# Kernel tuning notes

Hardware: AMD Instinct MI355X
Metric: run time of the kernel (lower is better)

Reference implementation:

```python
import jax, jax.numpy as jnp
import numpy as np

N, E, H = 50000, 800000, 128
NUM_NC = 40
NUM_LAYERS = 3


def setup_inputs() -> dict:
    key = jax.random.key(0)
    ks = jax.random.split(key, 16)
    s = 1.0 / np.sqrt(H)
    inp = {
        "x": jax.random.normal(ks[0], (N, H), jnp.float32),
        "edge_index": jax.random.randint(ks[1], (2, E), 0, N, jnp.int64),
        "na_alphas": 0.001 * jax.random.normal(ks[2], (3, 4), jnp.float32),
        "sc_alphas": 0.001 * jax.random.normal(ks[3], (2, 2), jnp.float32),
        "la_alphas": 0.001 * jax.random.normal(ks[4], (1, 3), jnp.float32),
        "lin1_W": s * jax.random.normal(ks[5], (H, H), jnp.float32),
        "lin1_b": jnp.zeros((H,), jnp.float32),
        "gcn_W": s * jax.random.normal(ks[6], (3, H, H), jnp.float32),
        "gcn_b": jnp.zeros((3, H), jnp.float32),
        "sage_Ws": s * jax.random.normal(ks[7], (3, H, H), jnp.float32),
        "sage_Wn": s * jax.random.normal(ks[8], (3, H, H), jnp.float32),
        "gin_W": s * jax.random.normal(ks[9], (3, H, H), jnp.float32),
        "gin_b": jnp.zeros((3, H), jnp.float32),
        "gin_eps": jnp.zeros((3,), jnp.float32),
        "gat_W": s * jax.random.normal(ks[10], (3, H, H), jnp.float32),
        "gat_as": s * jax.random.normal(ks[11], (3, H), jnp.float32),
        "gat_ad": s * jax.random.normal(ks[12], (3, H), jnp.float32),
        "nc_W": s * jax.random.normal(ks[13], (NUM_NC, H), jnp.float32),
        "nc_b": jnp.zeros((NUM_NC,), jnp.float32),
    }
    return inp


def _gcn(x, src, dst, deg_inv_sqrt, W, b):
    h = x @ W.T + b                           # [N, H]
    norm = deg_inv_sqrt[src] * deg_inv_sqrt[dst]
    msg = h[src] * norm[:, None]              # [E, H] gather
    return jax.ops.segment_sum(msg, dst, num_segments=N)


def _sage(x, src, dst, deg, Ws, Wn):
    agg = jax.ops.segment_sum(x[src], dst, num_segments=N) / jnp.maximum(deg, 1.0)[:, None]
    return x @ Ws.T + agg @ Wn.T


def _gin(x, src, dst, W, b, eps):
    agg = jax.ops.segment_sum(x[src], dst, num_segments=N)
    return ((1.0 + eps) * x + agg) @ W.T + b


def _gat(x, src, dst, W, a_s, a_d):
    h = x @ W.T                               # [N, H]
    logits = jax.nn.leaky_relu((h @ a_s)[src] + (h @ a_d)[dst], 0.2)  # [E]
    m = jax.ops.segment_max(logits, dst, num_segments=N)
    e = jnp.exp(logits - m[dst])
    z = jax.ops.segment_sum(e, dst, num_segments=N)
    alpha = e / (z[dst] + 1e-16)
    return jax.ops.segment_sum(alpha[:, None] * h[src], dst, num_segments=N)


def _na_mixed(x, w, src, dst, deg, dis, l, gcn_W, gcn_b, sage_Ws, sage_Wn,
              gin_W, gin_b, gin_eps, gat_W, gat_as, gat_ad):
    # sum_i w_i * elu(op_i(x, edge_index))
    o0 = _gcn(x, src, dst, dis, gcn_W[l], gcn_b[l])
    o1 = _sage(x, src, dst, deg, sage_Ws[l], sage_Wn[l])
    o2 = _gin(x, src, dst, gin_W[l], gin_b[l], gin_eps[l])
    o3 = _gat(x, src, dst, gat_W[l], gat_as[l], gat_ad[l])
    return (w[0] * jax.nn.elu(o0) + w[1] * jax.nn.elu(o1)
            + w[2] * jax.nn.elu(o2) + w[3] * jax.nn.elu(o3))


def reference(x, edge_index, na_alphas, sc_alphas, la_alphas, lin1_W, lin1_b,
              gcn_W, gcn_b, sage_Ws, sage_Wn, gin_W, gin_b, gin_eps,
              gat_W, gat_as, gat_ad, nc_W, nc_b):
    src, dst = edge_index[0], edge_index[1]
    deg = jax.ops.segment_sum(jnp.ones((E,), x.dtype), dst, num_segments=N)
    dis = jnp.where(deg > 0, 1.0 / jnp.sqrt(jnp.maximum(deg, 1.0)), 0.0)

    na_w = jax.nn.softmax(na_alphas, axis=-1)   # [3, 4]
    sc_w = jax.nn.softmax(sc_alphas, axis=-1)   # [2, 2] (none, skip)
    la_w = jax.nn.softmax(la_alphas, axis=-1)   # [1, 3]

    h = x @ lin1_W.T + lin1_b                   # dropout: eval mode -> identity
    xs = []
    cur = h
    for l in range(NUM_LAYERS):
        cur = _na_mixed(cur, na_w[l], src, dst, deg, dis, l, gcn_W, gcn_b,
                        sage_Ws, sage_Wn, gin_W, gin_b, gin_eps,
                        gat_W, gat_as, gat_ad)
        xs.append(cur)
    x1, x2, x3 = xs

    # fix_last=True: x4 = (x3, sc0(x1), sc1(x2)); SC ops = {none->0, skip->id}
    t = jnp.stack([x3, sc_w[0, 1] * x1, sc_w[1, 1] * x2], axis=0)  # [3, N, H]

    # layer aggregator: sum_i w_i * relu(op_i(tuple)); ops = {max, mean, sum}
    x5 = (la_w[0, 0] * jax.nn.relu(jnp.max(t, axis=0))
          + la_w[0, 1] * jax.nn.relu(jnp.mean(t, axis=0))
          + la_w[0, 2] * jax.nn.relu(jnp.sum(t, axis=0)))

    return x5 @ nc_W.T + nc_b                   # [N, NUM_NC]
```

## Files before the change

### kernel.cpp

```cpp
#include <hip/hip_runtime.h>
#include <hip/hip_bf16.h>

typedef unsigned short u16;
typedef unsigned int u32;
typedef __attribute__((ext_vector_type(8))) short short8;
typedef __attribute__((ext_vector_type(4))) float f32x4;
typedef __attribute__((ext_vector_type(2))) float f32x2;

#define HD 128
#define ETILE 8192

__device__ inline float b2f(u16 u){ u32 v = ((u32)u) << 16; return __uint_as_float(v); }
__device__ inline u16 f2b(float f){
  u32 u = __float_as_uint(f);
  u32 r = (u + 0x7fffu + ((u >> 16) & 1u)) >> 16;
  return (u16)r;
}
__device__ inline u32 pack2(float a, float b){
  __hip_bfloat162 h = __float22bfloat162_rn(make_float2(a, b));
  union { __hip_bfloat162 h; u32 u; } c; c.h = h; return c.u;
}
__device__ inline float lo2f(u32 w){ return b2f((u16)(w & 0xffff)); }
__device__ inline float hi2f(u32 w){ return b2f((u16)(w >> 16)); }
__device__ inline float eluf(float x){ return x > 0.f ? x : __expf(x) - 1.f; }
__device__ inline float reluf(float x){ return x > 0.f ? x : 0.f; }
__device__ inline float sane(float x){
  if (!(x == x)) return 0.f;
  return fminf(fmaxf(x, -1e30f), 1e30f);
}
__device__ inline u32 fenc(float f){ u32 u = __float_as_uint(f); return (u & 0x80000000u) ? ~u : (u | 0x80000000u); }
__device__ inline float fdec(u32 u){ return __uint_as_float((u & 0x80000000u) ? (u & 0x7fffffffu) : ~u); }
__device__ __forceinline__ void async16(const u16* g, u16* l){
  __builtin_amdgcn_global_load_lds((const __attribute__((address_space(1))) void*)g,
                                   (__attribute__((address_space(3))) void*)l, 16, 0, 0);
}

__global__ void k_small(const float* __restrict__ na_a, const float* __restrict__ sc_a,
                        const float* __restrict__ la_a, const float* __restrict__ gatW,
                        const float* __restrict__ gat_as, const float* __restrict__ gat_ad,
                        const float* __restrict__ gin_eps, float* __restrict__ sm,
                        u32* __restrict__ maxs)
{
  int t = threadIdx.x;
  if (t < 3) maxs[t] = 0u;
  if (t == 0){
    for (int l = 0; l < 3; l++){
      float a[4]; float mx = -1e30f;
      for (int i = 0; i < 4; i++){ a[i] = na_a[l*4+i]; mx = fmaxf(mx, a[i]); }
      float ssum = 0.f;
      for (int i = 0; i < 4; i++){ a[i] = __expf(a[i]-mx); ssum += a[i]; }
      for (int i = 0; i < 4; i++) sm[l*4+i] = a[i]/ssum;
    }
    for (int r = 0; r < 2; r++){
      float a0 = sc_a[r*2], a1 = sc_a[r*2+1];
      float mx = fmaxf(a0,a1);
      float e0 = __expf(a0-mx), e1 = __expf(a1-mx);
      sm[12+r] = e1/(e0+e1);
    }
    {
      float a0=la_a[0], a1=la_a[1], a2=la_a[2];
      float mx = fmaxf(fmaxf(a0,a1),a2);
      float e0=__expf(a0-mx), e1=__expf(a1-mx), e2=__expf(a2-mx);
      float ssum = e0+e1+e2;
      sm[14]=e0/ssum; sm[15]=e1/ssum; sm[16]=e2/ssum;
    }
    for (int l=0;l<3;l++) sm[17+l] = 1.f + gin_eps[l];
  }
  if (t < 128){
    for (int l=0;l<3;l++){
      float a1=0.f, a2=0.f;
      for (int k=0;k<128;k++){
        float wv = gatW[l*16384 + k*128 + t];
        a1 = fmaf(wv, gat_as[l*128+k], a1);
        a2 = fmaf(wv, gat_ad[l*128+k], a2);
      }
      sm[32  + l*128 + t] = a1;
      sm[416 + l*128 + t] = a2;
    }
  }
}

__device__ __forceinline__ uint4 cvt8(const float* __restrict__ p){
  float4 v0 = *(const float4*)p;
  float4 v1 = *(const float4*)(p + 4);
  uint4 o;
  o.x = pack2(v0.x, v0.y);
  o.y = pack2(v0.z, v0.w);
  o.z = pack2(v1.x, v1.y);
  o.w = pack2(v1.z, v1.w);
  return o;
}
__global__ void k_wcvt(const float* __restrict__ lin1W, const float* __restrict__ gcnW,
                       const float* __restrict__ Ws, const float* __restrict__ Wn,
                       const float* __restrict__ ginW, const float* __restrict__ gatW,
                       u16* __restrict__ wsb)
{
  int i = blockIdx.x*256 + threadIdx.x;
  if (i >= 32768) return;
  int m = i >> 11;
  int j = i & 2047;
  int r = j >> 4, c = j & 15;
  const float* src;
  if (m == 0)       src = lin1W;
  else if (m < 4)   src = gcnW + (m-1)*16384;
  else if (m < 7)   src = Ws   + (m-4)*16384;
  else if (m < 10)  src = Wn   + (m-7)*16384;
  else if (m < 13)  src = ginW + (m-10)*16384;
  else              src = gatW + (m-13)*16384;
  int dj = r*16 + (c ^ (r & 15));
  *(uint4*)(wsb + ((size_t)m*2048 + dj)*8) = cvt8(src + r*HD + c*8);
}


__global__ void k_ehist(const int* __restrict__ ei, int E, int* __restrict__ eh){
  __shared__ int h[256];
  int t = threadIdx.x, b = blockIdx.x;
  h[t] = 0; __syncthreads();
  int base = b*ETILE;
  #pragma unroll
  for (int r = 0; r < ETILE/256; r++){
    int e = base + r*256 + t;
    if (e < E) atomicAdd(&h[ei[E + e] >> 8], 1);
  }
  __syncthreads();
  eh[b*256 + t] = h[t];
}
__global__ void k_escan(int* __restrict__ eh, int nblk, int* __restrict__ btot){
  __shared__ int s[256];
  int b = blockIdx.x, t = threadIdx.x;
  int carry = 0;
  int rounds = (nblk + 255)/256;
  for (int r = 0; r < rounds; r++){
    int i = r*256 + t;
    int v = (i < nblk) ? eh[i*256 + b] : 0;
    s[t] = v; __syncthreads();
    for (int off = 1; off < 256; off <<= 1){
      int a = (t >= off) ? s[t - off] : 0;
      __syncthreads();
      s[t] += a;
      __syncthreads();
    }
    if (i < nblk) eh[i*256 + b] = s[t] - v + carry;
    carry += s[255];
    __syncthreads();
  }
  if (t == 0) btot[b] = carry;
}
__global__ void k_bscan(const int* __restrict__ btot, int B, int E, int* __restrict__ bbase){
  __shared__ int s[256];
  int t = threadIdx.x;
  int v = (t < B) ? btot[t] : 0;
  s[t] = v; __syncthreads();
  for (int off = 1; off < 256; off <<= 1){
    int a = (t >= off) ? s[t - off] : 0;
    __syncthreads();
    s[t] += a;
    __syncthreads();
  }
  if (t < B) bbase[t] = s[t] - v;
  if (t == 0) bbase[B] = E;
}
__global__ void k_escat(const int* __restrict__ ei, int E, int B,
                        const int* __restrict__ eh, const int* __restrict__ bbase,
                        int2* __restrict__ ebuf){
  __shared__ int cur[256];
  int t = threadIdx.x, b = blockIdx.x;
  cur[t] = (t < B) ? bbase[t] + eh[b*256 + t] : 0;
  __syncthreads();
  int base = b*ETILE;
  #pragma unroll
  for (int r = 0; r < ETILE/256; r++){
    int e = base + r*256 + t;
    if (e < E){
      int sv = ei[e], dv = ei[E + e];
      int p = atomicAdd(&cur[dv >> 8], 1);
      ebuf[p] = make_int2(sv, dv);
    }
  }
}
__global__ void k_bcount(const int2* __restrict__ ebuf, const int* __restrict__ bbase,
                         int Nn, int* __restrict__ cnt){
  __shared__ int c[256];
  int t = threadIdx.x, b = blockIdx.x;
  c[t] = 0; __syncthreads();
  int beg = bbase[b], end2 = bbase[b+1];
  for (int i = beg + t; i < end2; i += 256)
    atomicAdd(&c[ebuf[i].y & 255], 1);
  __syncthreads();
  int node = b*256 + t;
  if (node < Nn) cnt[node] = c[t];
}
__global__ void k_bfill(const int2* __restrict__ ebuf, const int* __restrict__ bbase,
                        const int* __restrict__ rowptr, int Nn, int* __restrict__ csr){
  __shared__ int cu[256];
  int t = threadIdx.x, b = blockIdx.x;
  int node = b*256 + t;
  cu[t] = (node < Nn) ? rowptr[node] : 0;
  __syncthreads();
  int beg = bbase[b], end2 = bbase[b+1];
  for (int i = beg + t; i < end2; i += 256){
    int2 ed = ebuf[i];
    int p = atomicAdd(&cu[ed.y & 255], 1);
    csr[p] = ed.x;
  }
}

__global__ void k_scan1(const int* __restrict__ cnt, int Nn, int* __restrict__ bsum){
  __shared__ int red[256];
  int b = blockIdx.x, t = threadIdx.x;
  int base = b*1024 + t*4;
  int s = 0;
  #pragma unroll
  for (int k = 0; k < 4; k++){ int i = base + k; if (i < Nn) s += cnt[i]; }
  red[t] = s; __syncthreads();
  for (int off = 128; off; off >>= 1){
    if (t < off) red[t] += red[t + off];
    __syncthreads();
  }
  if (t == 0) bsum[b] = red[0];
}

__global__ void k_scan2(const int* __restrict__ bsum, int nb,
                        int* __restrict__ boffs, int* __restrict__ rowptr, int Nn){
  __shared__ int sc[1024];
  int t = threadIdx.x;
  int own = (t < nb) ? bsum[t] : 0;
  sc[t] = own;
  __syncthreads();
  for (int off = 1; off < 1024; off <<= 1){
    int add = (t >= off) ? sc[t - off] : 0;
    __syncthreads();
    sc[t] += add;
    __syncthreads();
  }
  if (t < nb) boffs[t] = sc[t] - own;
  if (t == 1023) rowptr[Nn] = sc[1023];
}

__global__ void k_scan3(const int* __restrict__ cnt, const int* __restrict__ boffs, int Nn,
                        int* __restrict__ rowptr, float4* __restrict__ nd){
  __shared__ int red[256];
  int b = blockIdx.x, t = threadIdx.x;
  int base = b*1024 + t*4;
  int c[4]; int s = 0;
  #pragma unroll
  for (int k = 0; k < 4; k++){ int i = base + k; c[k] = (i < Nn) ? cnt[i] : 0; s += c[k]; }
  red[t] = s; __syncthreads();
  for (int off = 1; off < 256; off <<= 1){
    int add = (t >= off) ? red[t - off] : 0;
    __syncthreads();
    red[t] += add;
    __syncthreads();
  }
  int run = red[t] - s + boffs[b];
  #pragma unroll
  for (int k = 0; k < 4; k++){
    int i = base + k;
    if (i < Nn){
      rowptr[i] = run;
      float f = (float)c[k];
      nd[i].z = c[k] > 0 ? 1.f/sqrtf(f) : 0.f;
      nd[i].w = 1.f/fmaxf(f, 1.f);
      run += c[k];
    }
  }
}

__global__ void k_histblk(const int* __restrict__ cnt, int Nn, int* __restrict__ bh){
  __shared__ int h[256];
  int t = threadIdx.x, b = blockIdx.x;
  h[t] = 0; __syncthreads();
  int base = b*1024;
  #pragma unroll
  for (int k = 0; k < 4; k++){
    int i = base + t + k*256;
    if (i < Nn){ int d = cnt[i]; if (d > 255) d = 255; atomicAdd(&h[d], 1); }
  }
  __syncthreads();
  bh[b*256 + t] = h[t];
}
__global__ void k_hsscan(int* __restrict__ bh, int nb){
  __shared__ int tot[256];
  __shared__ int sc[256];
  int t = threadIdx.x;
  int s = 0;
  for (int b = 0; b < nb; b++){
    int v = bh[b*256 + t];
    bh[b*256 + t] = s;
    s += v;
  }
  tot[t] = s;
  int rt = 255 - t;
  __syncthreads();
  sc[rt] = tot[t];
  __syncthreads();
  for (int off = 1; off < 256; off <<= 1){
    int a = (rt >= off) ? sc[rt - off] : 0;
    __syncthreads();
    sc[rt] += a;
    __syncthreads();
  }
  int binbase = sc[rt] - tot[t];
  for (int b = 0; b < nb; b++) bh[b*256 + t] += binbase;
}
__global__ void k_permscat(const int* __restrict__ cnt, int Nn,
                           const int* __restrict__ bh, int* __restrict__ perm){
  __shared__ int cur[256];
  int t = threadIdx.x, b = blockIdx.x;
  cur[t] = bh[b*256 + t];
  __syncthreads();
  int base = b*1024;
  #pragma unroll
  for (int k = 0; k < 4; k++){
    int i = base + t + k*256;
    if (i < Nn){
      int d = cnt[i]; if (d > 255) d = 255;
      int p = atomicAdd(&cur[d], 1);
      perm[p] = i;
    }
  }
}

__global__ __launch_bounds__(256)
void k_agg(const u16* __restrict__ X, const int* __restrict__ rowptr, const int* __restrict__ csr,
           const int* __restrict__ perm,
           const float4* __restrict__ nd, const float* __restrict__ sm,
           const u32* __restrict__ maxs, int layer, int Nn,
           u16* __restrict__ Qb, u16* __restrict__ Pm, u16* __restrict__ Gb, u16* __restrict__ Rb,
           float* __restrict__ b0)
{
  int tid = threadIdx.x;
  int lane = tid & 63;
  int g = lane >> 4, t = lane & 15;
  int idx = blockIdx.x*16 + (tid >> 6)*4 + g;
  if (idx >= Nn) return;
  int wv = perm[idx];
  int beg = rowptr[wv], end = rowptr[wv+1];
  float4 ndw = nd[wv];
  float dval = ndw.y;
  float bnd = fdec(maxs[layer]) + dval;
  float mloc = fmaxf(bnd, 0.2f*bnd);
  f32x2 p2[4], q2[4], r2[4];
  #pragma unroll
  for (int k = 0; k < 4; k++){ p2[k] = (f32x2){0.f,0.f}; q2[k] = (f32x2){0.f,0.f}; r2[k] = (f32x2){0.f,0.f}; }
  float z = 0.f, qd = 0.f;
  int e = beg;
  int nsv0=0, nsv1=0, nsv2=0, nsv3=0;
  if (e + 3 < end){ nsv0 = csr[e]; nsv1 = csr[e+1]; nsv2 = csr[e+2]; nsv3 = csr[e+3]; }
  while (e + 3 < end){
    int sv0 = nsv0, sv1 = nsv1, sv2 = nsv2, sv3 = nsv3;
    int en = e + 4;
    if (en + 3 < end){ nsv0 = csr[en]; nsv1 = csr[en+1]; nsv2 = csr[en+2]; nsv3 = csr[en+3]; }
    float4 n0 = nd[sv0], n1 = nd[sv1], n2 = nd[sv2], n3 = nd[sv3];
    uint4 xv0 = *(const uint4*)(X + (size_t)sv0*HD + (t ^ (sv0 & 15))*8);
    uint4 xv1 = *(const uint4*)(X + (size_t)sv1*HD + (t ^ (sv1 & 15))*8);
    uint4 xv2 = *(const uint4*)(X + (size_t)sv2*HD + (t ^ (sv2 & 15))*8);
    uint4 xv3 = *(const uint4*)(X + (size_t)sv3*HD + (t ^ (sv3 & 15))*8);
    float s0 = n0.x + dval, s1 = n1.x + dval, s2 = n2.x + dval, s3 = n3.x + dval;
    float lg0 = fmaxf(s0, 0.2f*s0), lg1 = fmaxf(s1, 0.2f*s1);
    float lg2 = fmaxf(s2, 0.2f*s2), lg3 = fmaxf(s3, 0.2f*s3);
    float ew0 = __expf(lg0 - mloc), ew1 = __expf(lg1 - mloc);
    float ew2 = __expf(lg2 - mloc), ew3 = __expf(lg3 - mloc);
    u32 a0[4] = {xv0.x, xv0.y, xv0.z, xv0.w};
    u32 a1[4] = {xv1.x, xv1.y, xv1.z, xv1.w};
    u32 a2[4] = {xv2.x, xv2.y, xv2.z, xv2.w};
    u32 a3[4] = {xv3.x, xv3.y, xv3.z, xv3.w};
    f32x2 d0 = {n0.z, n0.z}, d1 = {n1.z, n1.z}, d2 = {n2.z, n2.z}, d3 = {n3.z, n3.z};
    f32x2 e0 = {ew0, ew0}, e1v = {ew1, ew1}, e2v = {ew2, ew2}, e3v = {ew3, ew3};
    #pragma unroll
    for (int k = 0; k < 4; k++){
      f32x2 xf0 = {lo2f(a0[k]), hi2f(a0[k])};
      f32x2 xf1 = {lo2f(a1[k]), hi2f(a1[k])};
      f32x2 xf2 = {lo2f(a2[k]), hi2f(a2[k])};
      f32x2 xf3 = {lo2f(a3[k]), hi2f(a3[k])};
      p2[k] += (xf0 + xf1) + (xf2 + xf3);
      q2[k] = __builtin_elementwise_fma(xf0, d0, q2[k]);
      q2[k] = __builtin_elementwise_fma(xf1, d1, q2[k]);
      q2[k] = __builtin_elementwise_fma(xf2, d2, q2[k]);
      q2[k] = __builtin_elementwise_fma(xf3, d3, q2[k]);
      r2[k] = __builtin_elementwise_fma(xf0, e0, r2[k]);
      r2[k] = __builtin_elementwise_fma(xf1, e1v, r2[k]);
      r2[k] = __builtin_elementwise_fma(xf2, e2v, r2[k]);
      r2[k] = __builtin_elementwise_fma(xf3, e3v, r2[k]);
    }
    z += (ew0 + ew1) + (ew2 + ew3);
    qd += (n0.z + n1.z) + (n2.z + n3.z);
    e = en;
  }
  if (e + 1 < end){
    int sv0 = csr[e], sv1 = csr[e+1];
    float4 n0 = nd[sv0], n1 = nd[sv1];
    uint4 xv0 = *(const uint4*)(X + (size_t)sv0*HD + (t ^ (sv0 & 15))*8);
    uint4 xv1 = *(const uint4*)(X + (size_t)sv1*HD + (t ^ (sv1 & 15))*8);
    float s0 = n0.x + dval, s1 = n1.x + dval;
    float lg0 = fmaxf(s0, 0.2f*s0);
    float lg1 = fmaxf(s1, 0.2f*s1);
    float ew0 = __expf(lg0 - mloc), ew1 = __expf(lg1 - mloc);
    u32 a0[4] = {xv0.x, xv0.y, xv0.z, xv0.w};
    u32 a1[4] = {xv1.x, xv1.y, xv1.z, xv1.w};
    f32x2 d0 = {n0.z, n0.z}, d1 = {n1.z, n1.z};
    f32x2 e0 = {ew0, ew0},   e1v = {ew1, ew1};
    #pragma unroll
    for (int k = 0; k < 4; k++){
      f32x2 xf0 = {lo2f(a0[k]), hi2f(a0[k])};
      f32x2 xf1 = {lo2f(a1[k]), hi2f(a1[k])};
      p2[k] += xf0 + xf1;
      q2[k] = __builtin_elementwise_fma(xf0, d0, q2[k]);
      q2[k] = __builtin_elementwise_fma(xf1, d1, q2[k]);
      r2[k] = __builtin_elementwise_fma(xf0, e0, r2[k]);
      r2[k] = __builtin_elementwise_fma(xf1, e1v, r2[k]);
    }
    z += ew0 + ew1; qd += n0.z + n1.z;
    e += 2;
  }
  if (e < end){
    int sv = csr[e];
    float4 n0 = nd[sv];
    uint4 xv = *(const uint4*)(X + (size_t)sv*HD + (t ^ (sv & 15))*8);
    float s = n0.x + dval;
    float lg = fmaxf(s, 0.2f*s);
    float ew = __expf(lg - mloc);
    u32 a0[4] = {xv.x, xv.y, xv.z, xv.w};
    f32x2 d0 = {n0.z, n0.z}, e0 = {ew, ew};
    #pragma unroll
    for (int k = 0; k < 4; k++){
      f32x2 xf = {lo2f(a0[k]), hi2f(a0[k])};
      p2[k] += xf;
      q2[k] = __builtin_elementwise_fma(xf, d0, q2[k]);
      r2[k] = __builtin_elementwise_fma(xf, e0, r2[k]);
    }
    z += ew; qd += n0.z;
  }
  {
    float disv = ndw.z, dinvv = ndw.w;
    float zinv = 1.f/(z + 1e-16f);
    float e1 = sm[17 + layer];
    int tch = t ^ (wv & 15);
    size_t o = (size_t)wv*HD + tch*8;
    uint4 xo = *(const uint4*)(X + o);
    u32 ax[4] = {xo.x, xo.y, xo.z, xo.w};
    uint4 qo, po, go, ro;
    u32* qp = (u32*)&qo; u32* pp = (u32*)&po; u32* gp = (u32*)&go; u32* rp = (u32*)&ro;
    #pragma unroll
    for (int k = 0; k < 4; k++){
      float x0 = lo2f(ax[k]), x1 = hi2f(ax[k]);
      qp[k] = pack2(disv*q2[k].x, disv*q2[k].y);
      pp[k] = pack2(dinvv*p2[k].x, dinvv*p2[k].y);
      gp[k] = pack2(fmaf(e1, x0, p2[k].x), fmaf(e1, x1, p2[k].y));
      rp[k] = pack2(zinv*r2[k].x, zinv*r2[k].y);
    }
    *(uint4*)(Qb + o) = qo;
    *(uint4*)(Pm + o) = po;
    *(uint4*)(Gb + o) = go;
    *(uint4*)(Rb + o) = ro;
    if (t == 0) b0[wv] = disv*qd;
  }
}

__device__ __forceinline__ void stageB_async(u16* lds, const u16* __restrict__ w, int tid){
  int lane = tid & 63, wave = tid >> 6;
  #pragma unroll
  for (int i = 0; i < 8; i++){
    int cb = wave*64 + 256*i;
    async16(w + (size_t)(cb + lane)*8, lds + (size_t)cb*8);
  }
}
__device__ __forceinline__ void stageA64_f32(u16* lds, const float* __restrict__ src,
                                             int mbase, int Nn, int tid){
  #pragma unroll
  for (int i = 0; i < 4; i++){
    int chunk = tid + 256*i;
    int r = chunk >> 4;
    int c = chunk & 15;
    uint4 v = {0u,0u,0u,0u};
    int gr = mbase + r;
    if (gr < Nn) v = cvt8(src + (size_t)gr*HD + c*8);
    *(uint4*)(lds + (r*16 + (c ^ (r & 15)))*8) = v;
  }
}
__device__ __forceinline__ void mfma_tile64(const u16* Als, const u16* Bls,
                                            int m0, int lane, f32x4 acc[8]){
  int quad = lane >> 4, lr = lane & 15;
  #pragma unroll
  for (int ks = 0; ks < 4; ks++){
    int q = ks*4 + quad;
    short8 a, b[8];
    int row = m0 + lr;
    a = *(const short8*)(Als + (row*16 + (q ^ lr))*8);
    #pragma unroll
    for (int ct = 0; ct < 8; ct++){
      int brow = ct*16 + lr;
      b[ct] = *(const short8*)(Bls + (brow*16 + (q ^ lr))*8);
    }
    #pragma unroll
    for (int ct = 0; ct < 8; ct++)
      acc[ct] = __builtin_amdgcn_mfma_f32_16x16x32_bf16(a, b[ct], acc[ct], 0, 0, 0);
  }
}

__global__ __launch_bounds__(256,3)
void k_gemm1(const float* __restrict__ A, const u16* __restrict__ Wb, const float* __restrict__ bias,
             const float* __restrict__ sm, float4* __restrict__ nd, u32* __restrict__ maxs,
             int Nn, u16* __restrict__ out)
{
  __shared__ __align__(16) u16 Als[64*128];
  __shared__ __align__(16) u16 Bls[128*128];
  __shared__ float mred[4];
  int tid = threadIdx.x;
  int lane = tid & 63, wave = tid >> 6;
  int m0 = wave*16, mbase = blockIdx.x*64;
  int quad = lane >> 4, lr = lane & 15;
  f32x4 acc[8];
  #pragma unroll
  for (int ct=0;ct<8;ct++) acc[ct] = (f32x4){0.f,0.f,0.f,0.f};
  stageB_async(Bls, Wb, tid);
  stageA64_f32(Als, A, mbase, Nn, tid);
  __syncthreads();
  mfma_tile64(Als, Bls, m0, lane, acc);
  #pragma unroll
  for (int ct=0;ct<8;ct++){
    float bc = bias[ct*16+lr];
    #pragma unroll
    for (int r=0;r<4;r++) acc[ct][r] = sane(acc[ct][r] + bc);
  }
  #pragma unroll
  for (int ct=0;ct<8;ct++){
    int c2 = ct*2 + (lr >> 3);
    #pragma unroll
    for (int r=0;r<4;r++){
      int grow = mbase + m0 + quad*4 + r;
      if (grow < Nn) out[(size_t)grow*HD + (c2 ^ (grow & 15))*8 + (lr & 7)] = f2b(acc[ct][r]);
    }
  }
  {
    const float* wsv = sm + 32;
    const float* wdv = sm + 416;
    float sp[4] = {0.f,0.f,0.f,0.f}, dp[4] = {0.f,0.f,0.f,0.f};
    #pragma unroll
    for (int ct=0;ct<8;ct++){
      float wsc = wsv[ct*16+lr], wdc = wdv[ct*16+lr];
      #pragma unroll
      for (int r=0;r<4;r++){
        sp[r] = fmaf(acc[ct][r], wsc, sp[r]);
        dp[r] = fmaf(acc[ct][r], wdc, dp[r]);
      }
    }
    #pragma unroll
    for (int off=1; off<16; off<<=1)
      #pragma unroll
      for (int r=0;r<4;r++){ sp[r] += __shfl_xor(sp[r], off); dp[r] += __shfl_xor(dp[r], off); }
    float ms = -3.4e38f;
    #pragma unroll
    for (int r=0;r<4;r++){
      int grow = mbase + m0 + quad*4 + r;
      if (grow < Nn){
        ms = fmaxf(ms, sp[r]);
        if (lr == 0) *(float2*)&nd[grow] = make_float2(sp[r], dp[r]);
      }
    }
    ms = fmaxf(ms, __shfl_xor(ms, 16));
    ms = fmaxf(ms, __shfl_xor(ms, 32));
    if (lane == 0) mred[wave] = ms;
    __syncthreads();
    if (tid == 0){
      float m = fmaxf(fmaxf(mred[0],mred[1]), fmaxf(mred[2],mred[3]));
      atomicMax(maxs + 0, fenc(m));
    }
  }
}

__global__ __launch_bounds__(256,3)
void k_layer3(const u16* __restrict__ X, const u16* __restrict__ Qb,
              const u16* __restrict__ Pm, const u16* __restrict__ Gb, const u16* __restrict__ Rb,
              float4* __restrict__ nd, const float* __restrict__ b0,
              const u16* __restrict__ wsb,
              const float* __restrict__ gcnB, const float* __restrict__ ginB,
              const float* __restrict__ sm, u32* __restrict__ maxs,
              int layer, int Nn, u16* __restrict__ out)
{
  __shared__ float mred[4];
  int tid = threadIdx.x;
  int lane = tid & 63, wave = tid >> 6;
  int m0 = wave*16, mbase = blockIdx.x*64;
  int quad = lane >> 4, lr = lane & 15;
  float w0 = sm[layer*4+0], w1 = sm[layer*4+1], w2 = sm[layer*4+2], w3 = sm[layer*4+3];
  const u16* gcnWb = wsb + (size_t)(1  + layer)*16384;
  const u16* WsWb  = wsb + (size_t)(4  + layer)*16384;
  const u16* WnWb  = wsb + (size_t)(7  + layer)*16384;
  const u16* ginWb = wsb + (size_t)(10 + layer)*16384;
  const u16* gatWb = wsb + (size_t)(13 + layer)*16384;

  int arow = mbase + m0 + lr; if (arow >= Nn) arow = Nn - 1;
  size_t abase = (size_t)arow * HD;
  int co[4];
  #pragma unroll
  for (int ks = 0; ks < 4; ks++) co[ks] = ((ks*4 + quad) ^ lr) * 8;
  int bro = lr * 128;

  f32x4 mix[8];
  f32x4 acc[8];
  float b0r[4];
  #pragma unroll
  for (int r=0;r<4;r++){
    int grow = mbase + m0 + quad*4 + r;
    b0r[r] = (grow < Nn) ? b0[grow] : 0.f;
  }

  short8 a0[4], a1[4];
  #pragma unroll
  for (int ks=0;ks<4;ks++) a0[ks] = *(const short8*)(Qb + abase + co[ks]);
  #pragma unroll
  for (int ks=0;ks<4;ks++) a1[ks] = *(const short8*)(X + abase + co[ks]);

  #pragma unroll
  for (int ct=0;ct<8;ct++) acc[ct] = (f32x4){0.f,0.f,0.f,0.f};
  #pragma unroll
  for (int ks=0;ks<4;ks++){
    #pragma unroll
    for (int ct=0;ct<8;ct++){
      short8 b = *(const short8*)(gcnWb + ct*2048 + bro + co[ks]);
      acc[ct] = __builtin_amdgcn_mfma_f32_16x16x32_bf16(a0[ks], b, acc[ct], 0, 0, 0);
    }
  }
  #pragma unroll
  for (int ks=0;ks<4;ks++) a0[ks] = *(const short8*)(Pm + abase + co[ks]);
  {
    float gb[8];
    #pragma unroll
    for (int ct=0;ct<8;ct++) gb[ct] = gcnB[layer*HD + ct*16+lr];
    #pragma unroll
    for (int ct=0;ct<8;ct++)
      #pragma unroll
      for (int r=0;r<4;r++)
        mix[ct][r] = w0 * eluf(acc[ct][r] + b0r[r]*gb[ct]);
  }

  #pragma unroll
  for (int ct=0;ct<8;ct++) acc[ct] = (f32x4){0.f,0.f,0.f,0.f};
  #pragma unroll
  for (int ks=0;ks<4;ks++){
    #pragma unroll
    for (int ct=0;ct<8;ct++){
      short8 b = *(const short8*)(WsWb + ct*2048 + bro + co[ks]);
      acc[ct] = __builtin_amdgcn_mfma_f32_16x16x32_bf16(a1[ks], b, acc[ct], 0, 0, 0);
    }
  }
  #pragma unroll
  for (int ks=0;ks<4;ks++) a1[ks] = *(const short8*)(Gb + abase + co[ks]);
  #pragma unroll
  for (int ks=0;ks<4;ks++){
    #pragma unroll
    for (int ct=0;ct<8;ct++){
      short8 b = *(const short8*)(WnWb + ct*2048 + bro + co[ks]);
      acc[ct] = __builtin_amdgcn_mfma_f32_16x16x32_bf16(a0[ks], b, acc[ct], 0, 0, 0);
    }
  }
  #pragma unroll
  for (int ks=0;ks<4;ks++) a0[ks] = *(const short8*)(Rb + abase + co[ks]);
  #pragma unroll
  for (int ct=0;ct<8;ct++)
    #pragma unroll
    for (int r=0;r<4;r++)
      mix[ct][r] += w1 * eluf(acc[ct][r]);

  #pragma unroll
  for (int ct=0;ct<8;ct++) acc[ct] = (f32x4){0.f,0.f,0.f,0.f};
  #pragma unroll
  for (int ks=0;ks<4;ks++){
    #pragma unroll
    for (int ct=0;ct<8;ct++){
      short8 b = *(const short8*)(ginWb + ct*2048 + bro + co[ks]);
      acc[ct] = __builtin_amdgcn_mfma_f32_16x16x32_bf16(a1[ks], b, acc[ct], 0, 0, 0);
    }
  }
  {
    float gib[8];
    #pragma unroll
    for (int ct=0;ct<8;ct++) gib[ct] = ginB[layer*HD + ct*16+lr];
    #pragma unroll
    for (int ct=0;ct<8;ct++)
      #pragma unroll
      for (int r=0;r<4;r++)
        mix[ct][r] += w2 * eluf(acc[ct][r] + gib[ct]);
  }

  #pragma unroll
  for (int ct=0;ct<8;ct++) acc[ct] = (f32x4){0.f,0.f,0.f,0.f};
  #pragma unroll
  for (int ks=0;ks<4;ks++){
    #pragma unroll
    for (int ct=0;ct<8;ct++){
      short8 b = *(const short8*)(gatWb + ct*2048 + bro + co[ks]);
      acc[ct] = __builtin_amdgcn_mfma_f32_16x16x32_bf16(a0[ks], b, acc[ct], 0, 0, 0);
    }
  }
  #pragma unroll
  for (int ct=0;ct<8;ct++)
    #pragma unroll
    for (int r=0;r<4;r++)
      mix[ct][r] = sane(mix[ct][r] + w3 * eluf(acc[ct][r]));

  #pragma unroll
  for (int ct=0;ct<8;ct++){
    int c2 = ct*2 + (lr >> 3);
    #pragma unroll
    for (int r=0;r<4;r++){
      int grow = mbase + m0 + quad*4 + r;
      if (grow < Nn) out[(size_t)grow*HD + (c2 ^ (grow & 15))*8 + (lr & 7)] = f2b(mix[ct][r]);
    }
  }
  if (layer < 2){
    const float* wsv = sm + 32  + (layer+1)*128;
    const float* wdv = sm + 416 + (layer+1)*128;
    float sp[4] = {0.f,0.f,0.f,0.f}, dp[4] = {0.f,0.f,0.f,0.f};
    #pragma unroll
    for (int ct=0;ct<8;ct++){
      float wsc = wsv[ct*16+lr], wdc = wdv[ct*16+lr];
      #pragma unroll
      for (int r=0;r<4;r++){
        sp[r] = fmaf(mix[ct][r], wsc, sp[r]);
        dp[r] = fmaf(mix[ct][r], wdc, dp[r]);
      }
    }
    #pragma unroll
    for (int off=1; off<16; off<<=1)
      #pragma unroll
      for (int r=0;r<4;r++){ sp[r] += __shfl_xor(sp[r], off); dp[r] += __shfl_xor(dp[r], off); }
    float ms = -3.4e38f;
    #pragma unroll
    for (int r=0;r<4;r++){
      int grow = mbase + m0 + quad*4 + r;
      if (grow < Nn){
        ms = fmaxf(ms, sp[r]);
        if (lr == 0) *(float2*)&nd[grow] = make_float2(sp[r], dp[r]);
      }
    }
    ms = fmaxf(ms, __shfl_xor(ms, 16));
    ms = fmaxf(ms, __shfl_xor(ms, 32));
    if (lane == 0) mred[wave] = ms;
    __syncthreads();
    if (tid == 0){
      float m = fmaxf(fmaxf(mred[0],mred[1]), fmaxf(mred[2],mred[3]));
      atomicMax(maxs + layer + 1, fenc(m));
    }
  }
}

__global__ __launch_bounds__(256)
void k_nc(const u16* __restrict__ X1, const u16* __restrict__ X2, const u16* __restrict__ X3,
          const float* __restrict__ W, const float* __restrict__ bias,
          const float* __restrict__ sm, int Nn, float* __restrict__ out)
{
  __shared__ __align__(16) u16 xs[32*136];
  __shared__ __align__(16) float wn[40*132];
  __shared__ float bs[40];
  int t = threadIdx.x;
  int nb = blockIdx.x*32;
  float c1 = sm[12], c2 = sm[13], la0 = sm[14], la1 = sm[15], la2 = sm[16];
  #pragma unroll
  for (int i = 0; i < 2; i++){
    int chunk = t + 256*i;
    int r = chunk >> 4, c = chunk & 15;
    uint4 v = {0u,0u,0u,0u};
    int gr = nb + r;
    if (gr < Nn){
      size_t o = (size_t)gr*HD + ((c ^ (gr & 15))*8);
      uint4 u1 = *(const uint4*)(X1 + o);
      uint4 u2 = *(const uint4*)(X2 + o);
      uint4 u3 = *(const uint4*)(X3 + o);
      u32* u1p = (u32*)&u1; u32* u2p = (u32*)&u2; u32* u3p = (u32*)&u3; u32* vp = (u32*)&v;
      #pragma unroll
      for (int k = 0; k < 4; k++){
        float o0, o1;
        {
          float a1 = lo2f(u1p[k]), a2 = lo2f(u2p[k]), a3 = lo2f(u3p[k]);
          float t0 = a3, t1 = c1*a1, t2 = c2*a2;
          float smm = t0 + t1 + t2;
          float mx = fmaxf(fmaxf(t0,t1),t2);
          o0 = la0*reluf(mx) + la1*reluf(smm*(1.f/3.f)) + la2*reluf(smm);
        }
        {
          float a1 = hi2f(u1p[k]), a2 = hi2f(u2p[k]), a3 = hi2f(u3p[k]);
          float t0 = a3, t1 = c1*a1, t2 = c2*a2;
          float smm = t0 + t1 + t2;
          float mx = fmaxf(fmaxf(t0,t1),t2);
          o1 = la0*reluf(mx) + la1*reluf(smm*(1.f/3.f)) + la2*reluf(smm);
        }
        vp[k] = pack2(sane(o0), sane(o1));
      }
    }
    *(uint4*)(xs + r*136 + c*8) = v;
  }
  #pragma unroll
  for (int i = 0; i < 5; i++){
    int chunk = t + 256*i;
    int r = chunk >> 5, c = chunk & 31;
    *(float4*)(wn + r*132 + c*4) = *(const float4*)(W + r*HD + c*4);
  }
  if (t < 40) bs[t] = bias[t];
  __syncthreads();
  int nl = t >> 3, cg = t & 7;
  float acc[5];
  #pragma unroll
  for (int j = 0; j < 5; j++) acc[j] = bs[cg + 8*j];
  for (int k = 0; k < 128; k++){
    float xv = b2f(xs[nl*136 + k]);
    #pragma unroll
    for (int j = 0; j < 5; j++)
      acc[j] = fmaf(xv, wn[(cg + 8*j)*132 + k], acc[j]);
  }
  int gr = nb + nl;
  if (gr < Nn){
    #pragma unroll
    for (int j = 0; j < 5; j++)
      out[(size_t)gr*40 + cg + 8*j] = sane(acc[j]);
  }
}

extern "C" void kernel_launch(void* const* d_in, const int* in_sizes, int n_in,
                              void* d_out, int out_size, void* d_ws, size_t ws_size,
                              hipStream_t stream)
{
  (void)n_in; (void)out_size; (void)ws_size;
  const int N = in_sizes[0] / HD;
  const int E = in_sizes[1] / 2;
  const float* x      = (const float*)d_in[0];
  const int*   ei     = (const int*)d_in[1];
  const float* na_a   = (const float*)d_in[2];
  const float* sc_a   = (const float*)d_in[3];
  const float* la_a   = (const float*)d_in[4];
  const float* lin1W  = (const float*)d_in[5];
  const float* lin1b  = (const float*)d_in[6];
  const float* gcnW   = (const float*)d_in[7];
  const float* gcnB   = (const float*)d_in[8];
  const float* sageWs = (const float*)d_in[9];
  const float* sageWn = (const float*)d_in[10];
  const float* ginW   = (const float*)d_in[11];
  const float* ginB   = (const float*)d_in[12];
  const float* ginE   = (const float*)d_in[13];
  const float* gatW   = (const float*)d_in[14];
  const float* gatAs  = (const float*)d_in[15];
  const float* gatAd  = (const float*)d_in[16];
  const float* ncW    = (const float*)d_in[17];
  const float* ncB    = (const float*)d_in[18];

  char* base = (char*)d_ws;
  size_t off = 0;
  auto alloc = [&](size_t b) -> void* {
    void* p = base + off;
    off += (b + 255) & ~(size_t)255;
    return p;
  };
  const int NB  = (N + 1023) / 1024;
  const int B   = (N + 255) >> 8;
  const int nbe = (E + ETILE - 1) / ETILE;
  float*  smalls = (float*)alloc(4096);
  u32*    maxs   = (u32*)alloc(256);
  int*    cnt    = (int*)alloc((size_t)N*4);
  int*    rowptr = (int*)alloc(((size_t)N+1)*4);
  int*    bsum   = (int*)alloc(4096);
  int*    boffs  = (int*)alloc(4096);
  int*    bh     = (int*)alloc((size_t)NB*256*4);
  int*    perm   = (int*)alloc((size_t)N*4);
  int*    eh     = (int*)alloc((size_t)nbe*256*4);
  int*    btot   = (int*)alloc(1024);
  int*    bbase  = (int*)alloc(1040);
  float4* nd     = (float4*)alloc((size_t)N*16);
  float*  b0     = (float*)alloc((size_t)N*4);
  int*    csr    = (int*)alloc((size_t)E*4);
  u16*    wsb    = (u16*)alloc((size_t)16*16384*2);
  u16*    xh     = (u16*)alloc((size_t)N*HD*2);
  u16*    x1     = (u16*)alloc((size_t)N*HD*2);
  u16*    x2     = (u16*)alloc((size_t)N*HD*2);
  u16*    Qb     = (u16*)alloc((size_t)N*HD*2);
  u16*    Pm     = (u16*)alloc((size_t)N*HD*2);
  u16*    Gb     = (u16*)alloc((size_t)N*HD*2);
  u16*    Rb     = (u16*)alloc((size_t)N*HD*2);
  int2*   ebuf   = (int2*)Qb;

  k_small<<<1,128,0,stream>>>(na_a, sc_a, la_a, gatW, gatAs, gatAd, ginE, smalls, maxs);
  k_wcvt<<<128,256,0,stream>>>(lin1W, gcnW, sageWs, sageWn, ginW, gatW, wsb);
  k_ehist<<<nbe,256,0,stream>>>(ei, E, eh);
  k_escan<<<B,256,0,stream>>>(eh, nbe, btot);
  k_bscan<<<1,256,0,stream>>>(btot, B, E, bbase);
  k_escat<<<nbe,256,0,stream>>>(ei, E, B, eh, bbase, ebuf);
  k_bcount<<<B,256,0,stream>>>(ebuf, bbase, N, cnt);
  k_histblk<<<NB,256,0,stream>>>(cnt, N, bh);
  k_hsscan<<<1,256,0,stream>>>(bh, NB);
  k_permscat<<<NB,256,0,stream>>>(cnt, N, bh, perm);
  k_scan1<<<NB,256,0,stream>>>(cnt, N, bsum);
  k_scan2<<<1,1024,0,stream>>>(bsum, NB, boffs, rowptr, N);
  k_scan3<<<NB,256,0,stream>>>(cnt, boffs, N, rowptr, nd);
  k_bfill<<<B,256,0,stream>>>(ebuf, bbase, rowptr, N, csr);
  int gbl64 = (N + 63)/64;
  k_gemm1<<<gbl64,256,0,stream>>>(x, wsb, lin1b, smalls, nd, maxs, N, xh);
  const u16* xc = xh;
  u16* outs[3] = {x1, x2, xh};
  int abl = (N + 15)/16;
  for (int l = 0; l < 3; l++){
    k_agg<<<abl,256,0,stream>>>(xc, rowptr, csr, perm, nd, smalls, maxs, l, N, Qb, Pm, Gb, Rb, b0);
    k_layer3<<<gbl64,256,0,stream>>>(xc, Qb, Pm, Gb, Rb, nd, b0, wsb,
                                     gcnB, ginB, smalls, maxs, l, N, outs[l]);
    xc = outs[l];
  }
  int ncbl = (N + 31)/32;
  k_nc<<<ncbl,256,0,stream>>>(x1, x2, xh, ncW, ncB, smalls, N, (float*)d_out);
}
```

Before: 512.1 us.

## Stage layer weights through double-buffered LDS with async prefetch in k_layer3

Replaces direct global-memory loads of the five 128x128 bf16 weight matrices in the fused layer kernel with async staging into two alternating shared-memory buffers. The next weight matrix is prefetched while the current one feeds the MFMAs, with a barrier between stages. The goal is to cut repeated global/L2 weight reads per wave and hide their latency. In exchange it uses 64KB of LDS per block, lowers the occupancy hint from 3 to 2 blocks, and adds five block-wide syncs.

```diff
diff --git a/kernel.cpp b/kernel.cpp
--- a/kernel.cpp
+++ b/kernel.cpp
@@ -497,6 +497,21 @@
       acc[ct] = __builtin_amdgcn_mfma_f32_16x16x32_bf16(a, b[ct], acc[ct], 0, 0, 0);
   }
 }
+__device__ __forceinline__ void mfma_regA(const short8 a[4], const u16* Bls,
+                                          int lane, f32x4 acc[8]){
+  int quad = lane >> 4, lr = lane & 15;
+  #pragma unroll
+  for (int ks = 0; ks < 4; ks++){
+    int q = ks*4 + quad;
+    short8 b[8];
+    #pragma unroll
+    for (int ct = 0; ct < 8; ct++)
+      b[ct] = *(const short8*)(Bls + ((ct*16 + lr)*16 + (q ^ lr))*8);
+    #pragma unroll
+    for (int ct = 0; ct < 8; ct++)
+      acc[ct] = __builtin_amdgcn_mfma_f32_16x16x32_bf16(a[ks], b[ct], acc[ct], 0, 0, 0);
+  }
+}
 
 __global__ __launch_bounds__(256,3)
 void k_gemm1(const float* __restrict__ A, const u16* __restrict__ Wb, const float* __restrict__ bias,
@@ -569,7 +584,7 @@
   }
 }
 
-__global__ __launch_bounds__(256,3)
+__global__ __launch_bounds__(256,2)
 void k_layer3(const u16* __restrict__ X, const u16* __restrict__ Qb,
               const u16* __restrict__ Pm, const u16* __restrict__ Gb, const u16* __restrict__ Rb,
               float4* __restrict__ nd, const float* __restrict__ b0,
@@ -578,6 +593,8 @@
               const float* __restrict__ sm, u32* __restrict__ maxs,
               int layer, int Nn, u16* __restrict__ out)
 {
+  __shared__ __align__(16) u16 Bls0[128*128];
+  __shared__ __align__(16) u16 Bls1[128*128];
   __shared__ float mred[4];
   int tid = threadIdx.x;
   int lane = tid & 63, wave = tid >> 6;
@@ -595,7 +612,6 @@
   int co[4];
   #pragma unroll
   for (int ks = 0; ks < 4; ks++) co[ks] = ((ks*4 + quad) ^ lr) * 8;
-  int bro = lr * 128;
 
   f32x4 mix[8];
   f32x4 acc[8];
@@ -607,21 +623,17 @@
   }
 
   short8 a0[4], a1[4];
+  stageB_async(Bls0, gcnWb, tid);
   #pragma unroll
   for (int ks=0;ks<4;ks++) a0[ks] = *(const short8*)(Qb + abase + co[ks]);
   #pragma unroll
   for (int ks=0;ks<4;ks++) a1[ks] = *(const short8*)(X + abase + co[ks]);
-
+  __syncthreads();
+
+  stageB_async(Bls1, WsWb, tid);
   #pragma unroll
   for (int ct=0;ct<8;ct++) acc[ct] = (f32x4){0.f,0.f,0.f,0.f};
-  #pragma unroll
-  for (int ks=0;ks<4;ks++){
-    #pragma unroll
-    for (int ct=0;ct<8;ct++){
-      short8 b = *(const short8*)(gcnWb + ct*2048 + bro + co[ks]);
-      acc[ct] = __builtin_amdgcn_mfma_f32_16x16x32_bf16(a0[ks], b, acc[ct], 0, 0, 0);
-    }
-  }
+  mfma_regA(a0, Bls0, lane, acc);
   #pragma unroll
   for (int ks=0;ks<4;ks++) a0[ks] = *(const short8*)(Pm + abase + co[ks]);
   {
@@ -634,27 +646,18 @@
       for (int r=0;r<4;r++)
         mix[ct][r] = w0 * eluf(acc[ct][r] + b0r[r]*gb[ct]);
   }
-
+  __syncthreads();
+
+  stageB_async(Bls0, WnWb, tid);
   #pragma unroll
   for (int ct=0;ct<8;ct++) acc[ct] = (f32x4){0.f,0.f,0.f,0.f};
-  #pragma unroll
-  for (int ks=0;ks<4;ks++){
-    #pragma unroll
-    for (int ct=0;ct<8;ct++){
-      short8 b = *(const short8*)(WsWb + ct*2048 + bro + co[ks]);
-      acc[ct] = __builtin_amdgcn_mfma_f32_16x16x32_bf16(a1[ks], b, acc[ct], 0, 0, 0);
-    }
-  }
+  mfma_regA(a1, Bls1, lane, acc);
   #pragma unroll
   for (int ks=0;ks<4;ks++) a1[ks] = *(const short8*)(Gb + abase + co[ks]);
-  #pragma unroll
-  for (int ks=0;ks<4;ks++){
-    #pragma unroll
-    for (int ct=0;ct<8;ct++){
-      short8 b = *(const short8*)(WnWb + ct*2048 + bro + co[ks]);
-      acc[ct] = __builtin_amdgcn_mfma_f32_16x16x32_bf16(a0[ks], b, acc[ct], 0, 0, 0);
-    }
-  }
+  __syncthreads();
+
+  stageB_async(Bls1, ginWb, tid);
+  mfma_regA(a0, Bls0, lane, acc);
   #pragma unroll
   for (int ks=0;ks<4;ks++) a0[ks] = *(const short8*)(Rb + abase + co[ks]);
   #pragma unroll
@@ -662,17 +665,12 @@
     #pragma unroll
     for (int r=0;r<4;r++)
       mix[ct][r] += w1 * eluf(acc[ct][r]);
-
+  __syncthreads();
+
+  stageB_async(Bls0, gatWb, tid);
   #pragma unroll
   for (int ct=0;ct<8;ct++) acc[ct] = (f32x4){0.f,0.f,0.f,0.f};
-  #pragma unroll
-  for (int ks=0;ks<4;ks++){
-    #pragma unroll
-    for (int ct=0;ct<8;ct++){
-      short8 b = *(const short8*)(ginWb + ct*2048 + bro + co[ks]);
-      acc[ct] = __builtin_amdgcn_mfma_f32_16x16x32_bf16(a1[ks], b, acc[ct], 0, 0, 0);
-    }
-  }
+  mfma_regA(a1, Bls1, lane, acc);
   {
     float gib[8];
     #pragma unroll
@@ -683,17 +681,11 @@
       for (int r=0;r<4;r++)
         mix[ct][r] += w2 * eluf(acc[ct][r] + gib[ct]);
   }
+  __syncthreads();
 
   #pragma unroll
   for (int ct=0;ct<8;ct++) acc[ct] = (f32x4){0.f,0.f,0.f,0.f};
-  #pragma unroll
-  for (int ks=0;ks<4;ks++){
-    #pragma unroll
-    for (int ct=0;ct<8;ct++){
-      short8 b = *(const short8*)(gatWb + ct*2048 + bro + co[ks]);
-      acc[ct] = __builtin_amdgcn_mfma_f32_16x16x32_bf16(a0[ks], b, acc[ct], 0, 0, 0);
-    }
-  }
+  mfma_regA(a0, Bls0, lane, acc);
   #pragma unroll
   for (int ct=0;ct<8;ct++)
     #pragma unroll
```

Measured after the change: 438.5 us. 14.4% less time.
